# Kernel optimization log

Hardware: AMD Instinct MI355X
Metric: run time of the kernel (lower is better)

The kernel has to match this reference:

```python
import jax, jax.numpy as jnp
import numpy as np

B, LENGTH, D, IN = 32, 32, 384, 384
NCELLS = LENGTH * (LENGTH + 1) // 2  # 528

def _offsets():
    off = np.zeros(LENGTH, dtype=np.int64)
    for lvl in range(1, LENGTH):
        off[lvl] = off[lvl - 1] + (LENGTH - (lvl - 1))
    return off

_OFF = _offsets()

def _inside_index(level):
    Ls = LENGTH - level
    pos = np.arange(Ls)[:, None]
    k = np.arange(level)[None, :]
    left = _OFF[k] + pos                      # span (k, pos)
    right = _OFF[level - k - 1] + pos + k + 1  # span (level-k-1, pos+k+1)
    return jnp.asarray(left), jnp.asarray(right)

def _outside_index(level):
    Ls = LENGTH - level
    N = LENGTH - level - 1  # constant #contexts per position
    par = np.zeros((Ls, N), dtype=np.int64)
    sib = np.zeros((Ls, N), dtype=np.int64)
    for pos in range(Ls):
        j = 0
        for s in range(LENGTH - pos - level - 1):  # node is left child
            par[pos, j] = _OFF[level + s + 1] + pos
            sib[pos, j] = _OFF[s] + pos + level + 1
            j += 1
        for s in range(pos):  # node is right child
            par[pos, j] = _OFF[level + s + 1] + pos - s - 1
            sib[pos, j] = _OFF[s] + pos - s - 1
            j += 1
    return jnp.asarray(par), jnp.asarray(sib)

def sigma_h(x):
    return x * jnp.tanh(jnp.sqrt(jax.nn.sigmoid(x)))

def layer_norm(x, g, b, eps=1e-5):
    mu = x.mean(-1, keepdims=True)
    var = ((x - mu) ** 2).mean(-1, keepdims=True)
    return (x - mu) * jax.lax.rsqrt(var + eps) * g + b

def compose(l, r, W0, W1, B0, W2, B1):
    h = sigma_h(l @ W0 + r @ W1 + B0)
    return sigma_h(h @ W2 + B1)

def bilinear(u, v, M):
    return jnp.einsum('blnd,de,blne->bln', u, M, v)[..., None]

def setup_inputs() -> dict:
    key = jax.random.key(0)
    ks = jax.random.split(key, 16)
    sc = 1.0 / np.sqrt(D)
    mk = lambda k, shp: (jax.random.normal(k, shp, dtype=jnp.float32) * sc)
    inp = {
        'x': jax.random.normal(ks[0], (B, LENGTH, IN), dtype=jnp.float32),
        'leaf_W': mk(ks[1], (IN, D)), 'leaf_b': jnp.zeros((D,), jnp.float32),
        'in_ln_g': jnp.ones((D,), jnp.float32), 'in_ln_b': jnp.zeros((D,), jnp.float32),
        'out_ln_g': jnp.ones((D,), jnp.float32), 'out_ln_b': jnp.zeros((D,), jnp.float32),
        'root_h': jax.random.normal(ks[2], (D,), dtype=jnp.float32) * 0.02,
        'in_bi': mk(ks[3], (D, D)), 'out_bi': mk(ks[4], (D, D)),
        'in_W0': mk(ks[5], (D, D)), 'in_W1': mk(ks[6], (D, D)),
        'in_B0': jnp.zeros((D,), jnp.float32),
        'in_W2': mk(ks[7], (D, D)), 'in_B1': jnp.zeros((D,), jnp.float32),
        'out_W0': mk(ks[8], (D, D)), 'out_W1': mk(ks[9], (D, D)),
        'out_B0': jnp.zeros((D,), jnp.float32),
        'out_W2': mk(ks[10], (D, D)), 'out_B1': jnp.zeros((D,), jnp.float32),
    }
    return inp

def reference(x, leaf_W, leaf_b, in_ln_g, in_ln_b, out_ln_g, out_ln_b, root_h,
              in_bi, out_bi, in_W0, in_W1, in_B0, in_W2, in_B1,
              out_W0, out_W1, out_B0, out_W2, out_B1):
    # leaf transform
    h0 = layer_norm(sigma_h(x @ leaf_W + leaf_b), in_ln_g, in_ln_b)
    ih = jnp.zeros((B, NCELLS, D), x.dtype).at[:, :LENGTH].set(h0)
    is_ = jnp.zeros((B, NCELLS, 1), x.dtype)
    # inside pass (CKY chart, level-by-level)
    for level in range(1, LENGTH):
        li, ri = _inside_index(level)
        lh, rh = ih[:, li], ih[:, ri]   # [B, Ls, level, D]
        ls, rs = is_[:, li], is_[:, ri]
        sc = bilinear(lh, rh, in_bi) + ls + rs
        p = jax.nn.softmax(sc, axis=2)
        xc = compose(lh, rh, in_W0, in_W1, in_B0, in_W2, in_B1)
        hbar = layer_norm((p * xc).sum(2), in_ln_g, in_ln_b)
        sbar = (p * sc).sum(2)
        o = int(_OFF[level]); Ls = LENGTH - level
        ih = ih.at[:, o:o + Ls].set(hbar)
        is_ = is_.at[:, o:o + Ls].set(sbar)
    # outside pass
    oh = jnp.zeros((B, NCELLS, D), x.dtype)
    os_ = jnp.zeros((B, NCELLS, 1), x.dtype)
    root = layer_norm(jnp.broadcast_to(root_h, (B, 1, D)), out_ln_g, out_ln_b)
    oh = oh.at[:, -1:].set(root)
    for level in range(LENGTH - 2, -1, -1):
        pi, si = _outside_index(level)
        ph, sh = oh[:, pi], ih[:, si]   # parent outside / sibling inside
        ps, ss = os_[:, pi], is_[:, si]
        sc = bilinear(sh, ph, out_bi) + ss + ps
        p = jax.nn.softmax(sc, axis=2)
        xc = compose(ph, sh, out_W0, out_W1, out_B0, out_W2, out_B1)
        hbar = layer_norm((p * xc).sum(2), out_ln_g, out_ln_b)
        sbar = (p * sc).sum(2)
        o = int(_OFF[level]); Ls = LENGTH - level
        oh = oh.at[:, o:o + Ls].set(hbar)
        os_ = os_.at[:, o:o + Ls].set(sbar)
    return ih, is_, oh, os_
```

## Files before the change

### kernel.cpp

```cpp
#include <hip/hip_runtime.h>
#include <cstddef>

#define BDIM 32
#define LEN 32
#define DD 384
#define NCELLS 528

typedef _Float16 h16;
typedef __attribute__((ext_vector_type(8))) _Float16 v8h;
typedef __attribute__((ext_vector_type(4))) float v4f;

__device__ __forceinline__ int offf(int k) { return k * 32 - ((k * (k - 1)) >> 1); }
static inline int offh(int k) { return k * 32 - ((k * (k - 1)) >> 1); }

__device__ __forceinline__ float sigma_h_f(float x) {
  float s = 1.0f / (1.0f + __expf(-x));
  float r = sqrtf(s);
  float e2 = __expf(2.0f * r);
  float th = 1.0f - 2.0f / (e2 + 1.0f);
  return x * th;
}

__device__ __forceinline__ size_t rowbase(int r, int gLs, int gOff) {
  if (gLs == 0) return (size_t)r;
  int b = r / gLs;
  int p = r - b * gLs;
  return (size_t)b * NCELLS + gOff + p;
}

__global__ __launch_bounds__(256) void pack3_k(
    const float* __restrict__ w0, const float* __restrict__ w1,
    const float* __restrict__ bi, const float* __restrict__ ow1,
    const float* __restrict__ obi, const float* __restrict__ w2,
    const float* __restrict__ ow2, const float* __restrict__ ow0,
    const float* __restrict__ lw,
    float* __restrict__ WCt, float* __restrict__ W2t, float* __restrict__ OW2t,
    float* __restrict__ OW0t, float* __restrict__ LWt,
    float* __restrict__ isp, float* __restrict__ osp) {
  int i = blockIdx.x * 256 + threadIdx.x;
  if (i < 1920 * 384) {
    int n = i / 384, k = i - n * 384;
    int sel = n / 384, c = n - sel * 384;
    const float* src = sel == 0 ? w0 : sel == 1 ? w1 : sel == 2 ? bi
                       : sel == 3 ? ow1 : obi;
    WCt[i] = src[k * 384 + c];
  }
  if (i < 384 * 384) {
    int n = i / 384, k = i - n * 384;
    W2t[i]  = w2[k * 384 + n];
    OW2t[i] = ow2[k * 384 + n];
    OW0t[i] = ow0[k * 384 + n];
    LWt[i]  = lw[k * 384 + n];
  }
  if (i < BDIM * NCELLS) { isp[i] = 0.0f; osp[i] = 0.0f; }
}

__global__ __launch_bounds__(256) void gemm32s(
    const float* __restrict__ A, const float* __restrict__ Wt,
    const float* __restrict__ bias, float* __restrict__ C,
    int M, int N, int act, int gLs, int gOff) {
  __shared__ h16 Ah[64][40], Al[64][40];
  __shared__ h16 Bh[128][40], Bl[128][40];
  int tid = threadIdx.x;
  int w = tid >> 6, lane = tid & 63;
  int m0 = blockIdx.x * 64, n0 = blockIdx.y * 128;
  int r = lane & 15, q = lane >> 4;

  v4f acc[4][2];
#pragma unroll
  for (int i = 0; i < 4; ++i)
#pragma unroll
    for (int j = 0; j < 2; ++j) acc[i][j] = (v4f){0.f, 0.f, 0.f, 0.f};

  int sar = tid >> 2;
  int sak = (tid & 3) << 3;
  const float* Aptr = nullptr;
  if (m0 + sar < M) Aptr = A + rowbase(m0 + sar, gLs, gOff) * (size_t)DD;
  int sbc = tid >> 1;
  int sbk = (tid & 1) << 4;
  const float* Bptr = Wt + (size_t)(n0 + sbc) * DD;

  for (int k0 = 0; k0 < DD; k0 += 32) {
    float4 a0 = make_float4(0.f, 0.f, 0.f, 0.f), a1 = a0;
    if (Aptr) {
      a0 = *reinterpret_cast<const float4*>(Aptr + k0 + sak);
      a1 = *reinterpret_cast<const float4*>(Aptr + k0 + sak + 4);
    }
    float4 b0 = *reinterpret_cast<const float4*>(Bptr + k0 + sbk);
    float4 b1 = *reinterpret_cast<const float4*>(Bptr + k0 + sbk + 4);
    float4 b2 = *reinterpret_cast<const float4*>(Bptr + k0 + sbk + 8);
    float4 b3 = *reinterpret_cast<const float4*>(Bptr + k0 + sbk + 12);
    __syncthreads();
    {
      float av[8] = {a0.x, a0.y, a0.z, a0.w, a1.x, a1.y, a1.z, a1.w};
      v8h hi, lo;
#pragma unroll
      for (int t = 0; t < 8; ++t) {
        h16 h = (h16)av[t];
        hi[t] = h;
        lo[t] = (h16)(av[t] - (float)h);
      }
      *reinterpret_cast<v8h*>(&Ah[sar][sak]) = hi;
      *reinterpret_cast<v8h*>(&Al[sar][sak]) = lo;
    }
    {
      float bv[16] = {b0.x, b0.y, b0.z, b0.w, b1.x, b1.y, b1.z, b1.w,
                      b2.x, b2.y, b2.z, b2.w, b3.x, b3.y, b3.z, b3.w};
      v8h hi0, lo0, hi1, lo1;
#pragma unroll
      for (int t = 0; t < 8; ++t) {
        h16 h = (h16)bv[t];
        hi0[t] = h;
        lo0[t] = (h16)(bv[t] - (float)h);
      }
#pragma unroll
      for (int t = 0; t < 8; ++t) {
        h16 h = (h16)bv[8 + t];
        hi1[t] = h;
        lo1[t] = (h16)(bv[8 + t] - (float)h);
      }
      *reinterpret_cast<v8h*>(&Bh[sbc][sbk]) = hi0;
      *reinterpret_cast<v8h*>(&Bl[sbc][sbk]) = lo0;
      *reinterpret_cast<v8h*>(&Bh[sbc][sbk + 8]) = hi1;
      *reinterpret_cast<v8h*>(&Bl[sbc][sbk + 8]) = lo1;
    }
    __syncthreads();
    v8h afh[4], afl[4], bfh[2], bfl[2];
#pragma unroll
    for (int i = 0; i < 4; ++i) {
      afh[i] = *reinterpret_cast<const v8h*>(&Ah[i * 16 + r][q * 8]);
      afl[i] = *reinterpret_cast<const v8h*>(&Al[i * 16 + r][q * 8]);
    }
#pragma unroll
    for (int j = 0; j < 2; ++j) {
      bfh[j] = *reinterpret_cast<const v8h*>(&Bh[w * 32 + j * 16 + r][q * 8]);
      bfl[j] = *reinterpret_cast<const v8h*>(&Bl[w * 32 + j * 16 + r][q * 8]);
    }
#pragma unroll
    for (int i = 0; i < 4; ++i)
#pragma unroll
      for (int j = 0; j < 2; ++j) {
        acc[i][j] = __builtin_amdgcn_mfma_f32_16x16x32_f16(afl[i], bfh[j], acc[i][j], 0, 0, 0);
        acc[i][j] = __builtin_amdgcn_mfma_f32_16x16x32_f16(afh[i], bfl[j], acc[i][j], 0, 0, 0);
        acc[i][j] = __builtin_amdgcn_mfma_f32_16x16x32_f16(afh[i], bfh[j], acc[i][j], 0, 0, 0);
      }
  }

#pragma unroll
  for (int i = 0; i < 4; ++i) {
#pragma unroll
    for (int reg = 0; reg < 4; ++reg) {
      int rr = m0 + i * 16 + q * 4 + reg;
      if (rr >= M) continue;
      size_t cb = rowbase(rr, gLs, gOff) * (size_t)N;
#pragma unroll
      for (int j = 0; j < 2; ++j) {
        int col = n0 + w * 32 + j * 16 + r;
        float v = acc[i][j][reg];
        if (bias) v += bias[col];
        if (act) v = sigma_h_f(v);
        C[cb + col] = v;
      }
    }
  }
}

__global__ __launch_bounds__(256) void k1_in(
    const float* __restrict__ PC, const float* __restrict__ ihp,
    float* __restrict__ isp, float* __restrict__ H, float* __restrict__ Pw,
    const float* __restrict__ B0, int L, int Ls, int offL) {
  int g = blockIdx.x;
  int b = g / Ls, pos = g - b * Ls;
  int tid = threadIdx.x, lane = tid & 63, wv = tid >> 6;
  __shared__ float scs[32];
  size_t cb = (size_t)b * NCELLS;
  for (int n = wv; n < L; n += 4) {
    int lc = offf(n) + pos;
    int rc = offf(L - 1 - n) + pos + n + 1;
    const float* u = PC + (cb + lc) * 1920 + 768;
    const float* v = ihp + (cb + rc) * (size_t)DD;
    float s = 0.0f;
#pragma unroll
    for (int jj = 0; jj < 6; ++jj) s += u[lane + 64 * jj] * v[lane + 64 * jj];
#pragma unroll
    for (int o = 32; o; o >>= 1) s += __shfl_xor(s, o, 64);
    if (lane == 0) scs[n] = s + isp[cb + lc] + isp[cb + rc];
  }
  __syncthreads();
  if (wv == 0) {
    float v = (lane < L) ? scs[lane] : -3.0e38f;
    float m = v;
#pragma unroll
    for (int o = 32; o; o >>= 1) m = fmaxf(m, __shfl_xor(m, o, 64));
    float e = (lane < L) ? __expf(v - m) : 0.0f;
    float S = e;
#pragma unroll
    for (int o = 32; o; o >>= 1) S += __shfl_xor(S, o, 64);
    float pn = e / S;
    if (lane < L) Pw[(size_t)g * L + lane] = pn;
    float sb = (lane < L) ? pn * v : 0.0f;
#pragma unroll
    for (int o = 32; o; o >>= 1) sb += __shfl_xor(sb, o, 64);
    if (lane == 0) isp[cb + offL + pos] = sb;
  }
  for (int n = 0; n < L; ++n) {
    int lc = offf(n) + pos;
    int rc = offf(L - 1 - n) + pos + n + 1;
    const float* A0r = PC + (cb + lc) * 1920;
    const float* A1r = PC + (cb + rc) * 1920 + 384;
    float* hrow = H + ((size_t)g * L + n) * DD;
    for (int k = tid; k < DD; k += 256)
      hrow[k] = sigma_h_f(A0r[k] + A1r[k] + B0[k]);
  }
}

__global__ __launch_bounds__(256) void k1_out(
    const float* __restrict__ PC, const float* __restrict__ P0,
    const float* __restrict__ ohp, const float* __restrict__ isp,
    float* __restrict__ osp, float* __restrict__ H, float* __restrict__ Pw,
    const float* __restrict__ B0, int L, int Ls, int Nc, int offL) {
  int g = blockIdx.x;
  int b = g / Ls, pos = g - b * Ls;
  int tid = threadIdx.x, lane = tid & 63, wv = tid >> 6;
  __shared__ float scs[32];
  size_t cb = (size_t)b * NCELLS;
  int cnt0 = 31 - pos - L;
  for (int j = wv; j < Nc; j += 4) {
    int par, sib;
    if (j < cnt0) { par = offf(L + j + 1) + pos; sib = offf(j) + pos + L + 1; }
    else { int s2 = j - cnt0; par = offf(L + s2 + 1) + pos - s2 - 1; sib = offf(s2) + pos - s2 - 1; }
    const float* u = PC + (cb + sib) * 1920 + 1536;
    const float* v = ohp + (cb + par) * (size_t)DD;
    float s = 0.0f;
#pragma unroll
    for (int jj = 0; jj < 6; ++jj) s += u[lane + 64 * jj] * v[lane + 64 * jj];
#pragma unroll
    for (int o = 32; o; o >>= 1) s += __shfl_xor(s, o, 64);
    if (lane == 0) scs[j] = s + isp[cb + sib] + osp[cb + par];
  }
  __syncthreads();
  if (wv == 0) {
    float v = (lane < Nc) ? scs[lane] : -3.0e38f;
    float m = v;
#pragma unroll
    for (int o = 32; o; o >>= 1) m = fmaxf(m, __shfl_xor(m, o, 64));
    float e = (lane < Nc) ? __expf(v - m) : 0.0f;
    float S = e;
#pragma unroll
    for (int o = 32; o; o >>= 1) S += __shfl_xor(S, o, 64);
    float pn = e / S;
    if (lane < Nc) Pw[(size_t)g * Nc + lane] = pn;
    float sb = (lane < Nc) ? pn * v : 0.0f;
#pragma unroll
    for (int o = 32; o; o >>= 1) sb += __shfl_xor(sb, o, 64);
    if (lane == 0) osp[cb + offL + pos] = sb;
  }
  for (int j = 0; j < Nc; ++j) {
    int par, sib;
    if (j < cnt0) { par = offf(L + j + 1) + pos; sib = offf(j) + pos + L + 1; }
    else { int s2 = j - cnt0; par = offf(L + s2 + 1) + pos - s2 - 1; sib = offf(s2) + pos - s2 - 1; }
    const float* p0r = P0 + (cb + par) * (size_t)DD;
    const float* s1r = PC + (cb + sib) * 1920 + 1152;
    float* hrow = H + ((size_t)g * Nc + j) * DD;
    for (int k = tid; k < DD; k += 256)
      hrow[k] = sigma_h_f(p0r[k] + s1r[k] + B0[k]);
  }
}

__global__ __launch_bounds__(128) void k3_red_ln(
    const float* __restrict__ XC, const float* __restrict__ Pw,
    const float* __restrict__ lng, const float* __restrict__ lnb,
    float* __restrict__ outArr, int L, int Ls, int offL) {
  int g = blockIdx.x;
  int b = g / Ls, pos = g - b * Ls;
  int tid = threadIdx.x;
  float a0 = 0, a1 = 0, a2 = 0;
  const float* base = XC + (size_t)g * L * DD;
  for (int n = 0; n < L; ++n) {
    float pw = Pw ? Pw[(size_t)g * L + n] : 1.0f;
    const float* row = base + (size_t)n * DD;
    a0 += pw * row[tid];
    a1 += pw * row[tid + 128];
    a2 += pw * row[tid + 256];
  }
  int lane = tid & 63, wv = tid >> 6;
  float s = a0 + a1 + a2;
#pragma unroll
  for (int o = 32; o; o >>= 1) s += __shfl_xor(s, o, 64);
  __shared__ float r1[2], r2[2];
  if (lane == 0) r1[wv] = s;
  __syncthreads();
  float mean = (r1[0] + r1[1]) * (1.0f / 384.0f);
  float d0 = a0 - mean, d1 = a1 - mean, d2 = a2 - mean;
  float q = d0 * d0 + d1 * d1 + d2 * d2;
#pragma unroll
  for (int o = 32; o; o >>= 1) q += __shfl_xor(q, o, 64);
  if (lane == 0) r2[wv] = q;
  __syncthreads();
  float var = (r2[0] + r2[1]) * (1.0f / 384.0f);
  float inv = rsqrtf(var + 1e-5f);
  float* out = outArr + ((size_t)b * NCELLS + offL + pos) * DD;
  out[tid]       = d0 * inv * lng[tid]       + lnb[tid];
  out[tid + 128] = d1 * inv * lng[tid + 128] + lnb[tid + 128];
  out[tid + 256] = d2 * inv * lng[tid + 256] + lnb[tid + 256];
}

__global__ __launch_bounds__(384) void root_k(
    const float* __restrict__ rooth, const float* __restrict__ lng,
    const float* __restrict__ lnb, const float* __restrict__ W0,
    float* __restrict__ ohp, float* __restrict__ P0) {
  int tid = threadIdx.x;
  int lane = tid & 63, wv = tid >> 6;
  __shared__ float rl[384];
  __shared__ float r1[6], r2[6];
  float x = rooth[tid];
  float s = x;
#pragma unroll
  for (int o = 32; o; o >>= 1) s += __shfl_xor(s, o, 64);
  if (lane == 0) r1[wv] = s;
  __syncthreads();
  float mean = (r1[0] + r1[1] + r1[2] + r1[3] + r1[4] + r1[5]) * (1.0f / 384.0f);
  float d = x - mean;
  float q = d * d;
#pragma unroll
  for (int o = 32; o; o >>= 1) q += __shfl_xor(q, o, 64);
  if (lane == 0) r2[wv] = q;
  __syncthreads();
  float var = (r2[0] + r2[1] + r2[2] + r2[3] + r2[4] + r2[5]) * (1.0f / 384.0f);
  float inv = rsqrtf(var + 1e-5f);
  float v = d * inv * lng[tid] + lnb[tid];
  rl[tid] = v;
  __syncthreads();
  for (int b2 = 0; b2 < BDIM; ++b2)
    ohp[((size_t)b2 * NCELLS + 527) * DD + tid] = v;
  float acc = 0.0f;
  for (int d2 = 0; d2 < 384; ++d2) acc += rl[d2] * W0[(size_t)d2 * 384 + tid];
  for (int b2 = 0; b2 < BDIM; ++b2)
    P0[((size_t)b2 * NCELLS + 527) * DD + tid] = acc;
}

extern "C" void kernel_launch(void* const* d_in, const int* in_sizes, int n_in,
                              void* d_out, int out_size, void* d_ws, size_t ws_size,
                              hipStream_t stream) {
  const float* x        = (const float*)d_in[0];
  const float* leaf_W   = (const float*)d_in[1];
  const float* leaf_b   = (const float*)d_in[2];
  const float* in_ln_g  = (const float*)d_in[3];
  const float* in_ln_b  = (const float*)d_in[4];
  const float* out_ln_g = (const float*)d_in[5];
  const float* out_ln_b = (const float*)d_in[6];
  const float* root_h   = (const float*)d_in[7];
  const float* in_bi    = (const float*)d_in[8];
  const float* out_bi   = (const float*)d_in[9];
  const float* in_W0    = (const float*)d_in[10];
  const float* in_W1    = (const float*)d_in[11];
  const float* in_B0    = (const float*)d_in[12];
  const float* in_W2    = (const float*)d_in[13];
  const float* in_B1    = (const float*)d_in[14];
  const float* out_W0   = (const float*)d_in[15];
  const float* out_W1   = (const float*)d_in[16];
  const float* out_B0   = (const float*)d_in[17];
  const float* out_W2   = (const float*)d_in[18];
  const float* out_B1   = (const float*)d_in[19];

  float* ih  = (float*)d_out;
  float* isp = ih + (size_t)BDIM * NCELLS * DD;
  float* oh  = isp + (size_t)BDIM * NCELLS;
  float* osp = oh + (size_t)BDIM * NCELLS * DD;

  float* PC   = (float*)d_ws;
  float* P0   = PC + (size_t)BDIM * NCELLS * 1920;
  float* XCb  = P0 + (size_t)BDIM * NCELLS * 384;
  float* Hbuf = XCb + (size_t)31744 * 384;
  float* Pw   = Hbuf + (size_t)31744 * 384;
  float* WCt  = Pw + 31744;
  float* W2t  = WCt + (size_t)1920 * 384;
  float* OW2t = W2t + (size_t)384 * 384;
  float* OW0t = OW2t + (size_t)384 * 384;
  float* LWt  = OW0t + (size_t)384 * 384;

  pack3_k<<<2880, 256, 0, stream>>>(in_W0, in_W1, in_bi, out_W1, out_bi,
                                    in_W2, out_W2, out_W0, leaf_W,
                                    WCt, W2t, OW2t, OW0t, LWt, isp, osp);

  gemm32s<<<dim3(16, 3), 256, 0, stream>>>(x, LWt, leaf_b, XCb, 1024, 384, 1, 0, 0);
  k3_red_ln<<<1024, 128, 0, stream>>>(XCb, nullptr, in_ln_g, in_ln_b, ih, 1, 32, 0);
  gemm32s<<<dim3(16, 15), 256, 0, stream>>>(ih, WCt, nullptr, PC, 1024, 1920, 0, 32, 0);

  for (int L = 1; L < LEN; ++L) {
    int Ls = LEN - L, G = BDIM * Ls, M = G * L, off = offh(L);
    k1_in<<<G, 256, 0, stream>>>(PC, ih, isp, Hbuf, Pw, in_B0, L, Ls, off);
    gemm32s<<<dim3((M + 63) / 64, 3), 256, 0, stream>>>(Hbuf, W2t, in_B1, XCb, M, 384, 1, 0, 0);
    k3_red_ln<<<G, 128, 0, stream>>>(XCb, Pw, in_ln_g, in_ln_b, ih, L, Ls, off);
    gemm32s<<<dim3((G + 63) / 64, 15), 256, 0, stream>>>(ih, WCt, nullptr, PC, G, 1920, 0, Ls, off);
  }

  root_k<<<1, 384, 0, stream>>>(root_h, out_ln_g, out_ln_b, out_W0, oh, P0);

  for (int L = LEN - 2; L >= 0; --L) {
    int Ls = LEN - L, Nc = LEN - 1 - L, G = BDIM * Ls, M = G * Nc, off = offh(L);
    k1_out<<<G, 256, 0, stream>>>(PC, P0, oh, isp, osp, Hbuf, Pw, out_B0, L, Ls, Nc, off);
    gemm32s<<<dim3((M + 63) / 64, 3), 256, 0, stream>>>(Hbuf, OW2t, out_B1, XCb, M, 384, 1, 0, 0);
    k3_red_ln<<<G, 128, 0, stream>>>(XCb, Pw, out_ln_g, out_ln_b, oh, Nc, Ls, off);
    if (L > 0)
      gemm32s<<<dim3((G + 63) / 64, 3), 256, 0, stream>>>(oh, OW0t, nullptr, P0, G, 384, 0, Ls, off);
  }
}
```

Baseline: 5.126 ms.

## Fuse score/softmax, first compose layer, second GEMM, weighted reduce and layernorm

Replaces the per-level k1 + gemm + k3_red_ln chain with a single fxc kernel. It computes bilinear scores and softmax, builds the sigma_h hidden rows directly into shared memory as split fp16 hi/lo, runs the W2 GEMM with MFMA, and reduces the weighted outputs via shared atomics before layernorm. This removes the large Hbuf/XC round-trips through global memory and two launches per level. W2 is pre-split into fp16 hi/lo at pack time, and the lo*lo product term is skipped. The cost is heavy LDS use (which limits occupancy), shared-memory atomics, and small grids at some levels.

```diff
diff --git a/kernel.cpp b/kernel.cpp
--- a/kernel.cpp
+++ b/kernel.cpp
@@ -28,14 +28,15 @@
   return (size_t)b * NCELLS + gOff + p;
 }
 
-__global__ __launch_bounds__(256) void pack3_k(
+__global__ __launch_bounds__(256) void pack4_k(
     const float* __restrict__ w0, const float* __restrict__ w1,
     const float* __restrict__ bi, const float* __restrict__ ow1,
     const float* __restrict__ obi, const float* __restrict__ w2,
     const float* __restrict__ ow2, const float* __restrict__ ow0,
     const float* __restrict__ lw,
-    float* __restrict__ WCt, float* __restrict__ W2t, float* __restrict__ OW2t,
-    float* __restrict__ OW0t, float* __restrict__ LWt,
+    float* __restrict__ WCt, float* __restrict__ OW0t, float* __restrict__ LWt,
+    h16* __restrict__ W2h, h16* __restrict__ W2l,
+    h16* __restrict__ OW2h, h16* __restrict__ OW2l,
     float* __restrict__ isp, float* __restrict__ osp) {
   int i = blockIdx.x * 256 + threadIdx.x;
   if (i < 1920 * 384) {
@@ -47,10 +48,14 @@
   }
   if (i < 384 * 384) {
     int n = i / 384, k = i - n * 384;
-    W2t[i]  = w2[k * 384 + n];
-    OW2t[i] = ow2[k * 384 + n];
     OW0t[i] = ow0[k * 384 + n];
     LWt[i]  = lw[k * 384 + n];
+    float v = w2[k * 384 + n];
+    h16 hh = (h16)v;
+    W2h[i] = hh; W2l[i] = (h16)(v - (float)hh);
+    v = ow2[k * 384 + n];
+    hh = (h16)v;
+    OW2h[i] = hh; OW2l[i] = (h16)(v - (float)hh);
   }
   if (i < BDIM * NCELLS) { isp[i] = 0.0f; osp[i] = 0.0f; }
 }
@@ -165,105 +170,239 @@
   }
 }
 
-__global__ __launch_bounds__(256) void k1_in(
-    const float* __restrict__ PC, const float* __restrict__ ihp,
-    float* __restrict__ isp, float* __restrict__ H, float* __restrict__ Pw,
-    const float* __restrict__ B0, int L, int Ls, int offL) {
-  int g = blockIdx.x;
-  int b = g / Ls, pos = g - b * Ls;
-  int tid = threadIdx.x, lane = tid & 63, wv = tid >> 6;
-  __shared__ float scs[32];
-  size_t cb = (size_t)b * NCELLS;
-  for (int n = wv; n < L; n += 4) {
-    int lc = offf(n) + pos;
-    int rc = offf(L - 1 - n) + pos + n + 1;
-    const float* u = PC + (cb + lc) * 1920 + 768;
-    const float* v = ihp + (cb + rc) * (size_t)DD;
-    float s = 0.0f;
-#pragma unroll
-    for (int jj = 0; jj < 6; ++jj) s += u[lane + 64 * jj] * v[lane + 64 * jj];
-#pragma unroll
-    for (int o = 32; o; o >>= 1) s += __shfl_xor(s, o, 64);
-    if (lane == 0) scs[n] = s + isp[cb + lc] + isp[cb + rc];
-  }
-  __syncthreads();
-  if (wv == 0) {
-    float v = (lane < L) ? scs[lane] : -3.0e38f;
+__global__ __launch_bounds__(256) void fxc(
+    const float* __restrict__ PC, const float* __restrict__ P0arr,
+    const float* __restrict__ vArr,
+    const float* __restrict__ sU, const float* __restrict__ sV,
+    float* __restrict__ outH, float* __restrict__ outS,
+    const h16* __restrict__ Wh, const h16* __restrict__ Wl,
+    const float* __restrict__ B0a, const float* __restrict__ B1a,
+    const float* __restrict__ lng, const float* __restrict__ lnb,
+    int mode, int L, int P, int Ls, int offL, int K) {
+  __shared__ h16 Ah[64][40], Al[64][40];
+  __shared__ h16 Bs[384][40];
+  __shared__ float hbar[8][388];
+  __shared__ float scs[64], pbuf[64];
+  __shared__ int posg[8], bg[8], rgl[64];
+
+  int tid = threadIdx.x;
+  int w = tid >> 6, lane = tid & 63;
+  int q = lane >> 4, r = lane & 15;
+  int blk = blockIdx.x;
+  int Gtot = BDIM * Ls;
+  int Kact = K; if (blk * K + Kact > Gtot) Kact = Gtot - blk * K;
+  int Mact = Kact * P;
+
+  if (tid < K) {
+    int g = blk * K + tid;
+    if (g < Gtot) { posg[tid] = g % Ls; bg[tid] = g / Ls; }
+  }
+  if (tid < 64) { pbuf[tid] = 0.0f; rgl[tid] = tid / P; }
+  for (int i = tid; i < 8 * 388; i += 256) ((float*)hbar)[i] = 0.0f;
+  __syncthreads();
+
+  for (int s = w; s < Mact; s += 4) {
+    int kg = s / P, n = s - kg * P;
+    int pos = posg[kg];
+    size_t cb = (size_t)bg[kg] * NCELLS;
+    int uc, vc;
+    if (mode == 0) {
+      uc = offf(n) + pos;
+      vc = offf(P - 1 - n) + pos + n + 1;
+    } else {
+      int cnt0 = 31 - pos - L;
+      if (n < cnt0) { vc = offf(L + n + 1) + pos; uc = offf(n) + pos + L + 1; }
+      else { int s2 = n - cnt0; vc = offf(L + s2 + 1) + pos - s2 - 1; uc = offf(s2) + pos - s2 - 1; }
+    }
+    const float* u = PC + (cb + uc) * 1920 + (mode ? 1536 : 768);
+    const float* vv = vArr + (cb + vc) * (size_t)DD;
+    float sdot = 0.0f;
+#pragma unroll
+    for (int jj = 0; jj < 6; ++jj) sdot += u[lane + 64 * jj] * vv[lane + 64 * jj];
+#pragma unroll
+    for (int o = 32; o; o >>= 1) sdot += __shfl_xor(sdot, o, 64);
+    if (lane == 0) scs[s] = sdot + sU[cb + uc] + sV[cb + vc];
+  }
+  __syncthreads();
+
+  for (int kg = w; kg < Kact; kg += 4) {
+    int base = kg * P;
+    float v = (lane < P) ? scs[base + lane] : -3.0e38f;
     float m = v;
 #pragma unroll
     for (int o = 32; o; o >>= 1) m = fmaxf(m, __shfl_xor(m, o, 64));
-    float e = (lane < L) ? __expf(v - m) : 0.0f;
+    float e = (lane < P) ? __expf(v - m) : 0.0f;
     float S = e;
 #pragma unroll
     for (int o = 32; o; o >>= 1) S += __shfl_xor(S, o, 64);
     float pn = e / S;
-    if (lane < L) Pw[(size_t)g * L + lane] = pn;
-    float sb = (lane < L) ? pn * v : 0.0f;
+    if (lane < P) pbuf[base + lane] = pn;
+    float sb = (lane < P) ? pn * v : 0.0f;
 #pragma unroll
     for (int o = 32; o; o >>= 1) sb += __shfl_xor(sb, o, 64);
-    if (lane == 0) isp[cb + offL + pos] = sb;
-  }
-  for (int n = 0; n < L; ++n) {
-    int lc = offf(n) + pos;
-    int rc = offf(L - 1 - n) + pos + n + 1;
-    const float* A0r = PC + (cb + lc) * 1920;
-    const float* A1r = PC + (cb + rc) * 1920 + 384;
-    float* hrow = H + ((size_t)g * L + n) * DD;
-    for (int k = tid; k < DD; k += 256)
-      hrow[k] = sigma_h_f(A0r[k] + A1r[k] + B0[k]);
-  }
-}
-
-__global__ __launch_bounds__(256) void k1_out(
-    const float* __restrict__ PC, const float* __restrict__ P0,
-    const float* __restrict__ ohp, const float* __restrict__ isp,
-    float* __restrict__ osp, float* __restrict__ H, float* __restrict__ Pw,
-    const float* __restrict__ B0, int L, int Ls, int Nc, int offL) {
-  int g = blockIdx.x;
-  int b = g / Ls, pos = g - b * Ls;
-  int tid = threadIdx.x, lane = tid & 63, wv = tid >> 6;
-  __shared__ float scs[32];
-  size_t cb = (size_t)b * NCELLS;
-  int cnt0 = 31 - pos - L;
-  for (int j = wv; j < Nc; j += 4) {
-    int par, sib;
-    if (j < cnt0) { par = offf(L + j + 1) + pos; sib = offf(j) + pos + L + 1; }
-    else { int s2 = j - cnt0; par = offf(L + s2 + 1) + pos - s2 - 1; sib = offf(s2) + pos - s2 - 1; }
-    const float* u = PC + (cb + sib) * 1920 + 1536;
-    const float* v = ohp + (cb + par) * (size_t)DD;
-    float s = 0.0f;
-#pragma unroll
-    for (int jj = 0; jj < 6; ++jj) s += u[lane + 64 * jj] * v[lane + 64 * jj];
-#pragma unroll
-    for (int o = 32; o; o >>= 1) s += __shfl_xor(s, o, 64);
-    if (lane == 0) scs[j] = s + isp[cb + sib] + osp[cb + par];
-  }
-  __syncthreads();
-  if (wv == 0) {
-    float v = (lane < Nc) ? scs[lane] : -3.0e38f;
-    float m = v;
-#pragma unroll
-    for (int o = 32; o; o >>= 1) m = fmaxf(m, __shfl_xor(m, o, 64));
-    float e = (lane < Nc) ? __expf(v - m) : 0.0f;
-    float S = e;
-#pragma unroll
-    for (int o = 32; o; o >>= 1) S += __shfl_xor(S, o, 64);
-    float pn = e / S;
-    if (lane < Nc) Pw[(size_t)g * Nc + lane] = pn;
-    float sb = (lane < Nc) ? pn * v : 0.0f;
-#pragma unroll
-    for (int o = 32; o; o >>= 1) sb += __shfl_xor(sb, o, 64);
-    if (lane == 0) osp[cb + offL + pos] = sb;
-  }
-  for (int j = 0; j < Nc; ++j) {
-    int par, sib;
-    if (j < cnt0) { par = offf(L + j + 1) + pos; sib = offf(j) + pos + L + 1; }
-    else { int s2 = j - cnt0; par = offf(L + s2 + 1) + pos - s2 - 1; sib = offf(s2) + pos - s2 - 1; }
-    const float* p0r = P0 + (cb + par) * (size_t)DD;
-    const float* s1r = PC + (cb + sib) * 1920 + 1152;
-    float* hrow = H + ((size_t)g * Nc + j) * DD;
-    for (int k = tid; k < DD; k += 256)
-      hrow[k] = sigma_h_f(p0r[k] + s1r[k] + B0[k]);
+    if (lane == 0) outS[(size_t)bg[kg] * NCELLS + offL + posg[kg]] = sb;
+  }
+  __syncthreads();
+
+  int srow = tid >> 2, skc = (tid & 3) << 3;
+  bool valid = srow < Mact;
+  const float* p1 = nullptr;
+  const float* p2 = nullptr;
+  if (valid) {
+    int kg = rgl[srow], n = srow - kg * P;
+    int pos = posg[kg];
+    size_t cb = (size_t)bg[kg] * NCELLS;
+    if (mode == 0) {
+      int lc = offf(n) + pos;
+      int rc = offf(P - 1 - n) + pos + n + 1;
+      p1 = PC + (cb + lc) * 1920;
+      p2 = PC + (cb + rc) * 1920 + 384;
+    } else {
+      int cnt0 = 31 - pos - L, par, sib;
+      if (n < cnt0) { par = offf(L + n + 1) + pos; sib = offf(n) + pos + L + 1; }
+      else { int s2 = n - cnt0; par = offf(L + s2 + 1) + pos - s2 - 1; sib = offf(s2) + pos - s2 - 1; }
+      p1 = P0arr + (cb + par) * (size_t)DD;
+      p2 = PC + (cb + sib) * 1920 + 1152;
+    }
+  }
+
+  v4f acc[4][6];
+#pragma unroll
+  for (int i = 0; i < 4; ++i)
+#pragma unroll
+    for (int jj = 0; jj < 6; ++jj) acc[i][jj] = (v4f){0.f, 0.f, 0.f, 0.f};
+
+  for (int k0 = 0; k0 < DD; k0 += 32) {
+    __syncthreads();
+    v8h hi = (v8h)(h16)0.f, lo = (v8h)(h16)0.f;
+    if (valid) {
+      float4 x0 = *reinterpret_cast<const float4*>(p1 + k0 + skc);
+      float4 x1 = *reinterpret_cast<const float4*>(p1 + k0 + skc + 4);
+      float4 y0 = *reinterpret_cast<const float4*>(p2 + k0 + skc);
+      float4 y1 = *reinterpret_cast<const float4*>(p2 + k0 + skc + 4);
+      float4 c0 = *reinterpret_cast<const float4*>(B0a + k0 + skc);
+      float4 c1 = *reinterpret_cast<const float4*>(B0a + k0 + skc + 4);
+      float e[8] = {x0.x + y0.x + c0.x, x0.y + y0.y + c0.y,
+                    x0.z + y0.z + c0.z, x0.w + y0.w + c0.w,
+                    x1.x + y1.x + c1.x, x1.y + y1.y + c1.y,
+                    x1.z + y1.z + c1.z, x1.w + y1.w + c1.w};
+#pragma unroll
+      for (int t = 0; t < 8; ++t) {
+        float h = sigma_h_f(e[t]);
+        h16 hh = (h16)h;
+        hi[t] = hh;
+        lo[t] = (h16)(h - (float)hh);
+      }
+    }
+    *reinterpret_cast<v8h*>(&Ah[srow][skc]) = hi;
+    *reinterpret_cast<v8h*>(&Al[srow][skc]) = lo;
+#pragma unroll
+    for (int i2 = 0; i2 < 6; ++i2) {
+      int c = tid + i2 * 256;
+      int n2 = c >> 2, kc2 = (c & 3) << 3;
+      *reinterpret_cast<v8h*>(&Bs[n2][kc2]) =
+          *reinterpret_cast<const v8h*>(Wh + (size_t)n2 * DD + k0 + kc2);
+    }
+    __syncthreads();
+    v8h afh[4], afl[4], bf[6];
+#pragma unroll
+    for (int i = 0; i < 4; ++i) {
+      afh[i] = *reinterpret_cast<const v8h*>(&Ah[i * 16 + r][q * 8]);
+      afl[i] = *reinterpret_cast<const v8h*>(&Al[i * 16 + r][q * 8]);
+    }
+#pragma unroll
+    for (int jj = 0; jj < 6; ++jj)
+      bf[jj] = *reinterpret_cast<const v8h*>(&Bs[w * 96 + jj * 16 + r][q * 8]);
+#pragma unroll
+    for (int i = 0; i < 4; ++i)
+#pragma unroll
+      for (int jj = 0; jj < 6; ++jj) {
+        acc[i][jj] = __builtin_amdgcn_mfma_f32_16x16x32_f16(afl[i], bf[jj], acc[i][jj], 0, 0, 0);
+        acc[i][jj] = __builtin_amdgcn_mfma_f32_16x16x32_f16(afh[i], bf[jj], acc[i][jj], 0, 0, 0);
+      }
+  }
+
+  for (int k0 = 0; k0 < DD; k0 += 32) {
+    __syncthreads();
+    v8h hi = (v8h)(h16)0.f;
+    if (valid) {
+      float4 x0 = *reinterpret_cast<const float4*>(p1 + k0 + skc);
+      float4 x1 = *reinterpret_cast<const float4*>(p1 + k0 + skc + 4);
+      float4 y0 = *reinterpret_cast<const float4*>(p2 + k0 + skc);
+      float4 y1 = *reinterpret_cast<const float4*>(p2 + k0 + skc + 4);
+      float4 c0 = *reinterpret_cast<const float4*>(B0a + k0 + skc);
+      float4 c1 = *reinterpret_cast<const float4*>(B0a + k0 + skc + 4);
+      float e[8] = {x0.x + y0.x + c0.x, x0.y + y0.y + c0.y,
+                    x0.z + y0.z + c0.z, x0.w + y0.w + c0.w,
+                    x1.x + y1.x + c1.x, x1.y + y1.y + c1.y,
+                    x1.z + y1.z + c1.z, x1.w + y1.w + c1.w};
+#pragma unroll
+      for (int t = 0; t < 8; ++t) hi[t] = (h16)sigma_h_f(e[t]);
+    }
+    *reinterpret_cast<v8h*>(&Ah[srow][skc]) = hi;
+#pragma unroll
+    for (int i2 = 0; i2 < 6; ++i2) {
+      int c = tid + i2 * 256;
+      int n2 = c >> 2, kc2 = (c & 3) << 3;
+      *reinterpret_cast<v8h*>(&Bs[n2][kc2]) =
+          *reinterpret_cast<const v8h*>(Wl + (size_t)n2 * DD + k0 + kc2);
+    }
+    __syncthreads();
+    v8h afh[4], bf[6];
+#pragma unroll
+    for (int i = 0; i < 4; ++i)
+      afh[i] = *reinterpret_cast<const v8h*>(&Ah[i * 16 + r][q * 8]);
+#pragma unroll
+    for (int jj = 0; jj < 6; ++jj)
+      bf[jj] = *reinterpret_cast<const v8h*>(&Bs[w * 96 + jj * 16 + r][q * 8]);
+#pragma unroll
+    for (int i = 0; i < 4; ++i)
+#pragma unroll
+      for (int jj = 0; jj < 6; ++jj)
+        acc[i][jj] = __builtin_amdgcn_mfma_f32_16x16x32_f16(afh[i], bf[jj], acc[i][jj], 0, 0, 0);
+  }
+
+  float b1v[6];
+#pragma unroll
+  for (int jj = 0; jj < 6; ++jj) b1v[jj] = B1a[w * 96 + jj * 16 + r];
+#pragma unroll
+  for (int i = 0; i < 4; ++i)
+#pragma unroll
+    for (int reg = 0; reg < 4; ++reg) {
+      int row = i * 16 + q * 4 + reg;
+      if (row < Mact) {
+        float pw = pbuf[row];
+        int kg = rgl[row];
+#pragma unroll
+        for (int jj = 0; jj < 6; ++jj) {
+          float v = sigma_h_f(acc[i][jj][reg] + b1v[jj]);
+          atomicAdd(&hbar[kg][w * 96 + jj * 16 + r], pw * v);
+        }
+      }
+    }
+  __syncthreads();
+
+  for (int kg = w; kg < Kact; kg += 4) {
+    float vals[6];
+    float sum = 0.0f;
+#pragma unroll
+    for (int jj = 0; jj < 6; ++jj) { vals[jj] = hbar[kg][lane + 64 * jj]; sum += vals[jj]; }
+#pragma unroll
+    for (int o = 32; o; o >>= 1) sum += __shfl_xor(sum, o, 64);
+    float mean = sum * (1.0f / 384.0f);
+    float qv = 0.0f;
+#pragma unroll
+    for (int jj = 0; jj < 6; ++jj) { float d = vals[jj] - mean; qv += d * d; }
+#pragma unroll
+    for (int o = 32; o; o >>= 1) qv += __shfl_xor(qv, o, 64);
+    float inv = rsqrtf(qv * (1.0f / 384.0f) + 1e-5f);
+    size_t cell = (size_t)bg[kg] * NCELLS + offL + posg[kg];
+    float* out = outH + cell * DD;
+#pragma unroll
+    for (int jj = 0; jj < 6; ++jj) {
+      int c = lane + 64 * jj;
+      out[c] = (vals[jj] - mean) * inv * lng[c] + lnb[c];
+    }
   }
 }
 
@@ -370,38 +509,43 @@
 
   float* PC   = (float*)d_ws;
   float* P0   = PC + (size_t)BDIM * NCELLS * 1920;
-  float* XCb  = P0 + (size_t)BDIM * NCELLS * 384;
-  float* Hbuf = XCb + (size_t)31744 * 384;
-  float* Pw   = Hbuf + (size_t)31744 * 384;
-  float* WCt  = Pw + 31744;
-  float* W2t  = WCt + (size_t)1920 * 384;
-  float* OW2t = W2t + (size_t)384 * 384;
-  float* OW0t = OW2t + (size_t)384 * 384;
+  float* WCt  = P0 + (size_t)BDIM * NCELLS * 384;
+  float* OW0t = WCt + (size_t)1920 * 384;
   float* LWt  = OW0t + (size_t)384 * 384;
-
-  pack3_k<<<2880, 256, 0, stream>>>(in_W0, in_W1, in_bi, out_W1, out_bi,
+  float* Lbuf = LWt + (size_t)384 * 384;
+  h16* W2h  = (h16*)(Lbuf + (size_t)1024 * 384);
+  h16* W2l  = W2h + (size_t)384 * 384;
+  h16* OW2h = W2l + (size_t)384 * 384;
+  h16* OW2l = OW2h + (size_t)384 * 384;
+
+  pack4_k<<<2880, 256, 0, stream>>>(in_W0, in_W1, in_bi, out_W1, out_bi,
                                     in_W2, out_W2, out_W0, leaf_W,
-                                    WCt, W2t, OW2t, OW0t, LWt, isp, osp);
-
-  gemm32s<<<dim3(16, 3), 256, 0, stream>>>(x, LWt, leaf_b, XCb, 1024, 384, 1, 0, 0);
-  k3_red_ln<<<1024, 128, 0, stream>>>(XCb, nullptr, in_ln_g, in_ln_b, ih, 1, 32, 0);
+                                    WCt, OW0t, LWt, W2h, W2l, OW2h, OW2l,
+                                    isp, osp);
+
+  gemm32s<<<dim3(16, 3), 256, 0, stream>>>(x, LWt, leaf_b, Lbuf, 1024, 384, 1, 0, 0);
+  k3_red_ln<<<1024, 128, 0, stream>>>(Lbuf, nullptr, in_ln_g, in_ln_b, ih, 1, 32, 0);
   gemm32s<<<dim3(16, 15), 256, 0, stream>>>(ih, WCt, nullptr, PC, 1024, 1920, 0, 32, 0);
 
   for (int L = 1; L < LEN; ++L) {
-    int Ls = LEN - L, G = BDIM * Ls, M = G * L, off = offh(L);
-    k1_in<<<G, 256, 0, stream>>>(PC, ih, isp, Hbuf, Pw, in_B0, L, Ls, off);
-    gemm32s<<<dim3((M + 63) / 64, 3), 256, 0, stream>>>(Hbuf, W2t, in_B1, XCb, M, 384, 1, 0, 0);
-    k3_red_ln<<<G, 128, 0, stream>>>(XCb, Pw, in_ln_g, in_ln_b, ih, L, Ls, off);
+    int P = L, Ls = LEN - L, G = BDIM * Ls, off = offh(L);
+    int K = (P < 8) ? 8 : (64 / P);
+    int Gk = (G + K - 1) / K;
+    fxc<<<Gk, 256, 0, stream>>>(PC, nullptr, ih, isp, isp, ih, isp,
+                                W2h, W2l, in_B0, in_B1, in_ln_g, in_ln_b,
+                                0, L, P, Ls, off, K);
     gemm32s<<<dim3((G + 63) / 64, 15), 256, 0, stream>>>(ih, WCt, nullptr, PC, G, 1920, 0, Ls, off);
   }
 
   root_k<<<1, 384, 0, stream>>>(root_h, out_ln_g, out_ln_b, out_W0, oh, P0);
 
   for (int L = LEN - 2; L >= 0; --L) {
-    int Ls = LEN - L, Nc = LEN - 1 - L, G = BDIM * Ls, M = G * Nc, off = offh(L);
-    k1_out<<<G, 256, 0, stream>>>(PC, P0, oh, isp, osp, Hbuf, Pw, out_B0, L, Ls, Nc, off);
-    gemm32s<<<dim3((M + 63) / 64, 3), 256, 0, stream>>>(Hbuf, OW2t, out_B1, XCb, M, 384, 1, 0, 0);
-    k3_red_ln<<<G, 128, 0, stream>>>(XCb, Pw, out_ln_g, out_ln_b, oh, Nc, Ls, off);
+    int P = LEN - 1 - L, Ls = LEN - L, G = BDIM * Ls, off = offh(L);
+    int K = (P < 8) ? 8 : (64 / P);
+    int Gk = (G + K - 1) / K;
+    fxc<<<Gk, 256, 0, stream>>>(PC, P0, oh, isp, osp, oh, osp,
+                                OW2h, OW2l, out_B0, out_B1, out_ln_g, out_ln_b,
+                                1, L, P, Ls, off, K);
     if (L > 0)
       gemm32s<<<dim3((G + 63) / 64, 3), 256, 0, stream>>>(oh, OW0t, nullptr, P0, G, 384, 0, Ls, off);
   }
```

Measured after the change: 7.320 ms. 42.8% more time.

## Pre-split hidden activations and W2 into fp16 hi/lo pairs for a dedicated GEMM

Applied to the files above, without the earlier changes.

The producer kernels (k1_in/k1_out) now write each hidden activation as an fp16 high/low pair instead of fp32, and the W2 weights are pre-split the same way at pack time. A new 128x128-tile MFMA GEMM (gemmsp) loads these pre-split halves directly, so the per-tile fp32-to-fp16 split inside the big per-level GEMM goes away. It also halves the number of row blocks and keeps the bias plus sigma_h epilogue. The cost is a larger accumulator tile, which raises register pressure, and fewer blocks on small levels.

```diff
diff --git a/kernel.cpp b/kernel.cpp
--- a/kernel.cpp
+++ b/kernel.cpp
@@ -28,14 +28,14 @@
   return (size_t)b * NCELLS + gOff + p;
 }
 
-__global__ __launch_bounds__(256) void pack3_k(
+__global__ __launch_bounds__(256) void pack5_k(
     const float* __restrict__ w0, const float* __restrict__ w1,
     const float* __restrict__ bi, const float* __restrict__ ow1,
     const float* __restrict__ obi, const float* __restrict__ w2,
     const float* __restrict__ ow2, const float* __restrict__ ow0,
     const float* __restrict__ lw,
-    float* __restrict__ WCt, float* __restrict__ W2t, float* __restrict__ OW2t,
-    float* __restrict__ OW0t, float* __restrict__ LWt,
+    float* __restrict__ WCt, float* __restrict__ OW0t, float* __restrict__ LWt,
+    h16* __restrict__ W2s, h16* __restrict__ OW2s,
     float* __restrict__ isp, float* __restrict__ osp) {
   int i = blockIdx.x * 256 + threadIdx.x;
   if (i < 1920 * 384) {
@@ -47,10 +47,16 @@
   }
   if (i < 384 * 384) {
     int n = i / 384, k = i - n * 384;
-    W2t[i]  = w2[k * 384 + n];
-    OW2t[i] = ow2[k * 384 + n];
     OW0t[i] = ow0[k * 384 + n];
     LWt[i]  = lw[k * 384 + n];
+    float v = w2[k * 384 + n];
+    h16 hh = (h16)v;
+    W2s[(size_t)n * 768 + k] = hh;
+    W2s[(size_t)n * 768 + 384 + k] = (h16)(v - (float)hh);
+    v = ow2[k * 384 + n];
+    hh = (h16)v;
+    OW2s[(size_t)n * 768 + k] = hh;
+    OW2s[(size_t)n * 768 + 384 + k] = (h16)(v - (float)hh);
   }
   if (i < BDIM * NCELLS) { isp[i] = 0.0f; osp[i] = 0.0f; }
 }
@@ -165,9 +171,88 @@
   }
 }
 
+__global__ __launch_bounds__(256) void gemmsp(
+    const h16* __restrict__ A, const h16* __restrict__ Wt,
+    const float* __restrict__ bias, float* __restrict__ C, int M) {
+  __shared__ h16 Ah[128][40], Al[128][40], Bh[128][40], Bl[128][40];
+  int tid = threadIdx.x;
+  int w = tid >> 6, lane = tid & 63;
+  int r = lane & 15, q = lane >> 4;
+  int m0 = blockIdx.x * 128, n0 = blockIdx.y * 128;
+
+  v4f acc[8][2];
+#pragma unroll
+  for (int i = 0; i < 8; ++i)
+#pragma unroll
+    for (int j = 0; j < 2; ++j) acc[i][j] = (v4f){0.f, 0.f, 0.f, 0.f};
+
+  int arow = tid >> 1;
+  int akc = (tid & 1) << 4;
+  const h16* Aptr = (m0 + arow < M) ? A + (size_t)(m0 + arow) * 768 : nullptr;
+  const h16* Bptr = Wt + (size_t)(n0 + arow) * 768;
+
+  for (int k0 = 0; k0 < DD; k0 += 32) {
+    v8h ah0 = (v8h)(h16)0.f, ah1 = ah0, al0 = ah0, al1 = ah0;
+    if (Aptr) {
+      ah0 = *reinterpret_cast<const v8h*>(Aptr + k0 + akc);
+      ah1 = *reinterpret_cast<const v8h*>(Aptr + k0 + akc + 8);
+      al0 = *reinterpret_cast<const v8h*>(Aptr + 384 + k0 + akc);
+      al1 = *reinterpret_cast<const v8h*>(Aptr + 384 + k0 + akc + 8);
+    }
+    v8h bh0 = *reinterpret_cast<const v8h*>(Bptr + k0 + akc);
+    v8h bh1 = *reinterpret_cast<const v8h*>(Bptr + k0 + akc + 8);
+    v8h bl0 = *reinterpret_cast<const v8h*>(Bptr + 384 + k0 + akc);
+    v8h bl1 = *reinterpret_cast<const v8h*>(Bptr + 384 + k0 + akc + 8);
+    __syncthreads();
+    *reinterpret_cast<v8h*>(&Ah[arow][akc])     = ah0;
+    *reinterpret_cast<v8h*>(&Ah[arow][akc + 8]) = ah1;
+    *reinterpret_cast<v8h*>(&Al[arow][akc])     = al0;
+    *reinterpret_cast<v8h*>(&Al[arow][akc + 8]) = al1;
+    *reinterpret_cast<v8h*>(&Bh[arow][akc])     = bh0;
+    *reinterpret_cast<v8h*>(&Bh[arow][akc + 8]) = bh1;
+    *reinterpret_cast<v8h*>(&Bl[arow][akc])     = bl0;
+    *reinterpret_cast<v8h*>(&Bl[arow][akc + 8]) = bl1;
+    __syncthreads();
+    v8h afh[8], afl[8], bfh[2], bfl[2];
+#pragma unroll
+    for (int i = 0; i < 8; ++i) {
+      afh[i] = *reinterpret_cast<const v8h*>(&Ah[i * 16 + r][q * 8]);
+      afl[i] = *reinterpret_cast<const v8h*>(&Al[i * 16 + r][q * 8]);
+    }
+#pragma unroll
+    for (int j = 0; j < 2; ++j) {
+      bfh[j] = *reinterpret_cast<const v8h*>(&Bh[w * 32 + j * 16 + r][q * 8]);
+      bfl[j] = *reinterpret_cast<const v8h*>(&Bl[w * 32 + j * 16 + r][q * 8]);
+    }
+#pragma unroll
+    for (int i = 0; i < 8; ++i)
+#pragma unroll
+      for (int j = 0; j < 2; ++j) {
+        acc[i][j] = __builtin_amdgcn_mfma_f32_16x16x32_f16(afl[i], bfh[j], acc[i][j], 0, 0, 0);
+        acc[i][j] = __builtin_amdgcn_mfma_f32_16x16x32_f16(afh[i], bfl[j], acc[i][j], 0, 0, 0);
+        acc[i][j] = __builtin_amdgcn_mfma_f32_16x16x32_f16(afh[i], bfh[j], acc[i][j], 0, 0, 0);
+      }
+  }
+
+#pragma unroll
+  for (int i = 0; i < 8; ++i) {
+#pragma unroll
+    for (int reg = 0; reg < 4; ++reg) {
+      int rr = m0 + i * 16 + q * 4 + reg;
+      if (rr >= M) continue;
+      size_t cb = (size_t)rr * DD;
+#pragma unroll
+      for (int j = 0; j < 2; ++j) {
+        int col = n0 + w * 32 + j * 16 + r;
+        C[cb + col] = sigma_h_f(acc[i][j][reg] + bias[col]);
+      }
+    }
+  }
+}
+
 __global__ __launch_bounds__(256) void k1_in(
     const float* __restrict__ PC, const float* __restrict__ ihp,
-    float* __restrict__ isp, float* __restrict__ H, float* __restrict__ Pw,
+    float* __restrict__ isp, h16* __restrict__ Hs, float* __restrict__ Pw,
     const float* __restrict__ B0, int L, int Ls, int offL) {
   int g = blockIdx.x;
   int b = g / Ls, pos = g - b * Ls;
@@ -208,16 +293,20 @@
     int rc = offf(L - 1 - n) + pos + n + 1;
     const float* A0r = PC + (cb + lc) * 1920;
     const float* A1r = PC + (cb + rc) * 1920 + 384;
-    float* hrow = H + ((size_t)g * L + n) * DD;
-    for (int k = tid; k < DD; k += 256)
-      hrow[k] = sigma_h_f(A0r[k] + A1r[k] + B0[k]);
+    h16* hrow = Hs + ((size_t)g * L + n) * 768;
+    for (int k = tid; k < DD; k += 256) {
+      float h = sigma_h_f(A0r[k] + A1r[k] + B0[k]);
+      h16 hh = (h16)h;
+      hrow[k] = hh;
+      hrow[384 + k] = (h16)(h - (float)hh);
+    }
   }
 }
 
 __global__ __launch_bounds__(256) void k1_out(
     const float* __restrict__ PC, const float* __restrict__ P0,
     const float* __restrict__ ohp, const float* __restrict__ isp,
-    float* __restrict__ osp, float* __restrict__ H, float* __restrict__ Pw,
+    float* __restrict__ osp, h16* __restrict__ Hs, float* __restrict__ Pw,
     const float* __restrict__ B0, int L, int Ls, int Nc, int offL) {
   int g = blockIdx.x;
   int b = g / Ls, pos = g - b * Ls;
@@ -261,9 +350,13 @@
     else { int s2 = j - cnt0; par = offf(L + s2 + 1) + pos - s2 - 1; sib = offf(s2) + pos - s2 - 1; }
     const float* p0r = P0 + (cb + par) * (size_t)DD;
     const float* s1r = PC + (cb + sib) * 1920 + 1152;
-    float* hrow = H + ((size_t)g * Nc + j) * DD;
-    for (int k = tid; k < DD; k += 256)
-      hrow[k] = sigma_h_f(p0r[k] + s1r[k] + B0[k]);
+    h16* hrow = Hs + ((size_t)g * Nc + j) * 768;
+    for (int k = tid; k < DD; k += 256) {
+      float h = sigma_h_f(p0r[k] + s1r[k] + B0[k]);
+      h16 hh = (h16)h;
+      hrow[k] = hh;
+      hrow[384 + k] = (h16)(h - (float)hh);
+    }
   }
 }
 
@@ -371,26 +464,27 @@
   float* PC   = (float*)d_ws;
   float* P0   = PC + (size_t)BDIM * NCELLS * 1920;
   float* XCb  = P0 + (size_t)BDIM * NCELLS * 384;
-  float* Hbuf = XCb + (size_t)31744 * 384;
-  float* Pw   = Hbuf + (size_t)31744 * 384;
+  float* Pw   = XCb + (size_t)31744 * 384;
   float* WCt  = Pw + 31744;
-  float* W2t  = WCt + (size_t)1920 * 384;
-  float* OW2t = W2t + (size_t)384 * 384;
-  float* OW0t = OW2t + (size_t)384 * 384;
+  float* OW0t = WCt + (size_t)1920 * 384;
   float* LWt  = OW0t + (size_t)384 * 384;
-
-  pack3_k<<<2880, 256, 0, stream>>>(in_W0, in_W1, in_bi, out_W1, out_bi,
+  float* Lbuf = LWt + (size_t)384 * 384;
+  h16* Hs   = (h16*)(Lbuf + (size_t)1024 * 384);
+  h16* W2s  = Hs + (size_t)31744 * 768;
+  h16* OW2s = W2s + (size_t)384 * 768;
+
+  pack5_k<<<2880, 256, 0, stream>>>(in_W0, in_W1, in_bi, out_W1, out_bi,
                                     in_W2, out_W2, out_W0, leaf_W,
-                                    WCt, W2t, OW2t, OW0t, LWt, isp, osp);
-
-  gemm32s<<<dim3(16, 3), 256, 0, stream>>>(x, LWt, leaf_b, XCb, 1024, 384, 1, 0, 0);
-  k3_red_ln<<<1024, 128, 0, stream>>>(XCb, nullptr, in_ln_g, in_ln_b, ih, 1, 32, 0);
+                                    WCt, OW0t, LWt, W2s, OW2s, isp, osp);
+
+  gemm32s<<<dim3(16, 3), 256, 0, stream>>>(x, LWt, leaf_b, Lbuf, 1024, 384, 1, 0, 0);
+  k3_red_ln<<<1024, 128, 0, stream>>>(Lbuf, nullptr, in_ln_g, in_ln_b, ih, 1, 32, 0);
   gemm32s<<<dim3(16, 15), 256, 0, stream>>>(ih, WCt, nullptr, PC, 1024, 1920, 0, 32, 0);
 
   for (int L = 1; L < LEN; ++L) {
     int Ls = LEN - L, G = BDIM * Ls, M = G * L, off = offh(L);
-    k1_in<<<G, 256, 0, stream>>>(PC, ih, isp, Hbuf, Pw, in_B0, L, Ls, off);
-    gemm32s<<<dim3((M + 63) / 64, 3), 256, 0, stream>>>(Hbuf, W2t, in_B1, XCb, M, 384, 1, 0, 0);
+    k1_in<<<G, 256, 0, stream>>>(PC, ih, isp, Hs, Pw, in_B0, L, Ls, off);
+    gemmsp<<<dim3((M + 127) / 128, 3), 256, 0, stream>>>(Hs, W2s, in_B1, XCb, M);
     k3_red_ln<<<G, 128, 0, stream>>>(XCb, Pw, in_ln_g, in_ln_b, ih, L, Ls, off);
     gemm32s<<<dim3((G + 63) / 64, 15), 256, 0, stream>>>(ih, WCt, nullptr, PC, G, 1920, 0, Ls, off);
   }
@@ -399,8 +493,8 @@
 
   for (int L = LEN - 2; L >= 0; --L) {
     int Ls = LEN - L, Nc = LEN - 1 - L, G = BDIM * Ls, M = G * Nc, off = offh(L);
-    k1_out<<<G, 256, 0, stream>>>(PC, P0, oh, isp, osp, Hbuf, Pw, out_B0, L, Ls, Nc, off);
-    gemm32s<<<dim3((M + 63) / 64, 3), 256, 0, stream>>>(Hbuf, OW2t, out_B1, XCb, M, 384, 1, 0, 0);
+    k1_out<<<G, 256, 0, stream>>>(PC, P0, oh, isp, osp, Hs, Pw, out_B0, L, Ls, Nc, off);
+    gemmsp<<<dim3((M + 127) / 128, 3), 256, 0, stream>>>(Hs, OW2s, out_B1, XCb, M);
     k3_red_ln<<<G, 128, 0, stream>>>(XCb, Pw, out_ln_g, out_ln_b, oh, Nc, Ls, off);
     if (L > 0)
       gemm32s<<<dim3((G + 63) / 64, 3), 256, 0, stream>>>(oh, OW0t, nullptr, P0, G, 384, 0, Ls, off);
```

After: 5.359 ms. +4.5%, slower.
